# Kernel tuning notes

Hardware: AMD Instinct MI355X
Metric: run time of the kernel (lower is better)

The kernel has to match this reference:

```python
import jax, jax.numpy as jnp
import numpy as np

D = 1024      # input_dim = clip_model.text_projection.shape[1]
P = D // 8    # pre_dim1 == pre_dim2 == 128
B, NS, NT, C = 4096, 8192, 8192, 1000
EPS = 1e-5
SCALE = 0.1
BETA_S = 1.0
BETA_T = 1.0


def setup_inputs() -> dict:
    key = jax.random.key(0)
    ks = jax.random.split(key, 24)
    rn = lambda k, shp, s=0.02: jax.random.normal(k, shp, dtype=jnp.float32) * s
    inp = {
        "Ft": jax.random.normal(ks[0], (C, D), dtype=jnp.float32),
        "Fv": jax.random.normal(ks[1], (B, D), dtype=jnp.float32),
        "Fvs_bank": jax.random.normal(ks[2], (NS, D), dtype=jnp.float32),
        "Fvt_bank": jax.random.normal(ks[3], (NT, D), dtype=jnp.float32),
        # pre_project: Linear(D->P), BN(P), ReLU, Linear(P->P), BN(P), ReLU, Linear(P->3D)
        "W1": rn(ks[4], (P, D)), "b1": jnp.zeros((P,), jnp.float32),
        "g1": jnp.ones((P,), jnp.float32), "be1": jnp.zeros((P,), jnp.float32),
        "m1": jnp.zeros((P,), jnp.float32), "v1": jnp.ones((P,), jnp.float32),
        "W2": rn(ks[5], (P, P)), "b2": jnp.zeros((P,), jnp.float32),
        "g2": jnp.ones((P,), jnp.float32), "be2": jnp.zeros((P,), jnp.float32),
        "m2": jnp.zeros((P,), jnp.float32), "v2": jnp.ones((P,), jnp.float32),
        "W3": rn(ks[6], (3 * D, P)), "b3": jnp.zeros((3 * D,), jnp.float32),
        # post_project: Linear(D->D)
        "Wp": rn(ks[7], (D, D)), "bp": jnp.zeros((D,), jnp.float32),
        "logit_scale": jnp.asarray(np.log(1.0 / 0.07), dtype=jnp.float32),
    }
    return inp


def _pre_project(x, W1, b1, g1, be1, m1, v1, W2, b2, g2, be2, m2, v2, W3, b3):
    # Linear -> BatchNorm1d (eval: running stats) -> ReLU, twice, then Linear to 3*D
    h = x @ W1.T + b1
    h = jax.nn.relu((h - m1) * jax.lax.rsqrt(v1 + EPS) * g1 + be1)
    h = h @ W2.T + b2
    h = jax.nn.relu((h - m2) * jax.lax.rsqrt(v2 + EPS) * g2 + be2)
    return h @ W3.T + b3  # (n, 3*D)


def _qkv(o):
    # einops 'b (d k) -> k b d' with k=3: interleaved split along last dim
    o = o.reshape(o.shape[0], D, 3)
    return o[..., 0], o[..., 1], o[..., 2]


def reference(Ft, Fv, Fvs_bank, Fvt_bank, W1, b1, g1, be1, m1, v1,
              W2, b2, g2, be2, m2, v2, W3, b3, Wp, bp, logit_scale):
    pre = lambda x: _pre_project(x, W1, b1, g1, be1, m1, v1,
                                 W2, b2, g2, be2, m2, v2, W3, b3)
    q_fv, _, _ = _qkv(pre(Fv))
    _, k_fvs, v_fvs = _qkv(pre(Fvs_bank))
    _, k_fvt, v_fvt = _qkv(pre(Fvt_bank))

    As = jax.nn.softmax(SCALE * (q_fv @ k_fvs.T), axis=-1)  # (B, NS)
    At = jax.nn.softmax(SCALE * (q_fv @ k_fvt.T), axis=-1)  # (B, NT)

    Fsa = Fv + (As @ v_fvs) @ Wp.T + bp
    Fta = Fv + (At @ v_fvt) @ Wp.T + bp
    Fsa = Fsa / jnp.linalg.norm(Fsa, axis=-1, keepdims=True)
    Fta = Fta / jnp.linalg.norm(Fta, axis=-1, keepdims=True)

    ls = jnp.exp(logit_scale)
    logits = BETA_S * ls * (Fsa @ Ft.T) + BETA_T * ls * (Fta @ Ft.T)
    return logits  # (B, C)
```

## Files before the change

### kernel.cpp

```cpp
#include <hip/hip_runtime.h>
#include <hip/hip_bf16.h>
#include <math.h>

#define D_DIM   1024
#define P_DIM   128
#define B_ROWS  4096
#define NBANK   8192
#define C_CLS   1000
#define EPS_BN  1e-5f
#define SCALE_S 0.1f
#define MTOT    20480
#define KVSEG   8
#define KCH     64
#define CHUNKS  (NBANK / KVSEG / KCH)

typedef __bf16 bf16x8 __attribute__((ext_vector_type(8)));
typedef float  f32x4  __attribute__((ext_vector_type(4)));
typedef __hip_bfloat16 bf;

__device__ __forceinline__ void load_lds16(const void* gp, void* lp) {
    __builtin_amdgcn_global_load_lds(
        (__attribute__((address_space(1))) void*)gp,
        (__attribute__((address_space(3))) void*)lp, 16, 0, 0);
}

__device__ __forceinline__ int4 pack8(float4 a, float4 b) {
    union { bf h[8]; int4 v; } u;
    u.h[0] = __float2bfloat16(a.x); u.h[1] = __float2bfloat16(a.y);
    u.h[2] = __float2bfloat16(a.z); u.h[3] = __float2bfloat16(a.w);
    u.h[4] = __float2bfloat16(b.x); u.h[5] = __float2bfloat16(b.y);
    u.h[6] = __float2bfloat16(b.z); u.h[7] = __float2bfloat16(b.w);
    return u.v;
}

__global__ __launch_bounds__(256)
void gemm_bf16(const bf* __restrict__ A, const bf* __restrict__ B,
               int M, int N, int K, int lda, int ldb,
               int kchunks, int fx, int fy, int epi,
               float* __restrict__ Cf, bf* __restrict__ Cb,
               const float* __restrict__ bias, const float* __restrict__ biasm,
               const float* __restrict__ bng, const float* __restrict__ bnb,
               const float* __restrict__ bnm, const float* __restrict__ bnv,
               const float* __restrict__ addsrc, const float* __restrict__ lsp,
               int ldc)
{
    __shared__ __align__(16) short ldsS[8192];
    short* lsA = ldsS;
    short* lsB = ldsS + 4096;

    const int tid  = threadIdx.x;
    const int wave = tid >> 6;
    const int lane = tid & 63;
    const int wm   = wave >> 1;
    const int wn   = wave & 1;
    const int r16  = lane & 15;
    const int quad = lane >> 4;

    const int gx = gridDim.x, gy = gridDim.y;
    const int l   = blockIdx.y * gx + blockIdx.x;
    const int xcd = l & 7;
    const int i0  = l >> 3;
    const int sx  = gx / fx, sy = gy / fy;
    const int bx  = (xcd % fx) * sx + (i0 % sx);
    const int by  = (xcd / fx) * sy + (i0 / sx);
    const int bm0 = by * 128;
    const int bn0 = bx * 128;

    const int kper = K / kchunks;
    const int kbeg = blockIdx.z * kper;
    const int kend = kbeg + kper;

    f32x4 acc[4][4];
#pragma unroll
    for (int i = 0; i < 4; ++i)
#pragma unroll
        for (int j = 0; j < 4; ++j) acc[i][j] = (f32x4){0.f, 0.f, 0.f, 0.f};

    for (int k0 = kbeg; k0 < kend; k0 += 32) {
#pragma unroll
        for (int i = 0; i < 2; ++i) {
            const int s   = i * 256 + tid;
            const int row = s >> 2;
            const int cc  = (s & 3) * 8;
            const int lofs = (i * 256 + wave * 64) * 16;
            load_lds16(A + (size_t)(bm0 + row) * lda + k0 + cc, (char*)lsA + lofs);
            load_lds16(B + (size_t)(bn0 + row) * ldb + k0 + cc, (char*)lsB + lofs);
        }
        __syncthreads();

        bf16x8 af[4], bfr[4];
#pragma unroll
        for (int i = 0; i < 4; ++i)
            af[i] = *(const bf16x8*)(lsA + (wm * 64 + i * 16 + r16) * 32 + quad * 8);
#pragma unroll
        for (int j = 0; j < 4; ++j)
            bfr[j] = *(const bf16x8*)(lsB + (wn * 64 + j * 16 + r16) * 32 + quad * 8);
#pragma unroll
        for (int i = 0; i < 4; ++i)
#pragma unroll
            for (int j = 0; j < 4; ++j)
                acc[i][j] = __builtin_amdgcn_mfma_f32_16x16x32_bf16(
                    af[i], bfr[j], acc[i][j], 0, 0, 0);
        __syncthreads();
    }

    if (epi == 3 || epi == 4) {
        const float lsv = (epi == 4) ? expf(*lsp) : 1.0f;
#pragma unroll
        for (int i = 0; i < 4; ++i) {
            const int gmb = bm0 + wm * 64 + i * 16 + quad * 4;
#pragma unroll
            for (int j = 0; j < 4; ++j) {
                const int gn = bn0 + wn * 64 + j * 16 + r16;
#pragma unroll
                for (int r = 0; r < 4; ++r) {
                    const int gm = gmb + r;
                    float val = acc[i][j][r];
                    if (epi == 3) {
                        Cf[(size_t)gm * N + gn] =
                            val + bias[gn] + addsrc[(size_t)(gm & (ldc - 1)) * N + gn];
                    } else {
                        if (gn < ldc) Cf[(size_t)gm * ldc + gn] = val * lsv;
                    }
                }
            }
        }
        return;
    }

    bf* dst = Cb + (epi == 6 ? (size_t)blockIdx.z * M * N : 0);
    bf* my  = (bf*)(ldsS + wave * 2048);

#pragma unroll
    for (int half = 0; half < 2; ++half) {
#pragma unroll
        for (int i2 = 0; i2 < 2; ++i2) {
            const int i = half * 2 + i2;
            const int gmb = bm0 + wm * 64 + i * 16 + quad * 4;
#pragma unroll
            for (int j = 0; j < 4; ++j) {
                const int gn = bn0 + wn * 64 + j * 16 + r16;
#pragma unroll
                for (int r = 0; r < 4; ++r) {
                    float val = acc[i][j][r];
                    if (epi == 1) {
                        val += bias[gn];
                        val = (val - bnm[gn]) * rsqrtf(bnv[gn] + EPS_BN) * bng[gn] + bnb[gn];
                        val = fmaxf(val, 0.f);
                    } else {
                        if (bias)  val += bias[gn];
                        if (biasm) val += biasm[gmb + r];
                    }
                    my[(i2 * 16 + quad * 4 + r) * 64 + j * 16 + r16] =
                        __float2bfloat16(val);
                }
            }
        }
#pragma unroll
        for (int it = 0; it < 4; ++it) {
            const int chunk = it * 64 + lane;
            const int lrow  = chunk >> 3;
            const int lcol  = (chunk & 7) * 8;
            const int grow  = bm0 + wm * 64 + half * 32 + lrow;
            const int gcol  = bn0 + wn * 64 + lcol;
            int4 v = *(const int4*)(my + lrow * 64 + lcol);
            *(int4*)(dst + (size_t)grow * N + gcol) = v;
        }
    }
}

__global__ __launch_bounds__(256)
void attn_fused(const bf* __restrict__ qt,
                const bf* __restrict__ h2bank,
                const bf* __restrict__ h2T,
                const float* __restrict__ beta,
                bf* __restrict__ Ypart,
                float* __restrict__ rsP)
{
    __shared__ __align__(16) short lds[40960];
    short* lsQ = lds;
    short* lsK = lds + 16384;
    short* lsV = lds + 24576;
    short* lsS = lds + 32768;

    const int tid  = threadIdx.x;
    const int wave = tid >> 6;
    const int lane = tid & 63;
    const int wm   = wave >> 1;
    const int wn   = wave & 1;
    const int r16  = lane & 15;
    const int quad = lane >> 4;

    const int qb   = blockIdx.x >> 4;
    const int side = (blockIdx.x >> 3) & 1;
    const int seg  = blockIdx.x & 7;
    const int part = side * 8 + seg;
    const int nseg0 = seg * (NBANK / KVSEG);
    const bf* kbase = h2bank + (size_t)side * NBANK * P_DIM;
    const int ncol0 = side * NBANK;

#pragma unroll
    for (int m = 0; m < 8; ++m) {
        const int s = m * 256 + tid;
        const int row = s >> 4, pcg = s & 15;
        const int lcg = pcg ^ (row & 15);
        load_lds16(qt + (size_t)(qb * 128 + row) * 128 + lcg * 8,
                   (char*)lsQ + (m * 256 + wave * 64) * 16);
    }

    f32x4 sacc[4][2], yacc[4][4];
    float rsacc[4][4];
#pragma unroll
    for (int i = 0; i < 4; ++i) {
#pragma unroll
        for (int j = 0; j < 4; ++j) yacc[i][j] = (f32x4){0.f, 0.f, 0.f, 0.f};
#pragma unroll
        for (int j = 0; j < 2; ++j) sacc[i][j] = (f32x4){0.f, 0.f, 0.f, 0.f};
#pragma unroll
        for (int r = 0; r < 4; ++r) rsacc[i][r] = 0.f;
    }

    for (int c = 0; c < CHUNKS; ++c) {
        const int kv0 = nseg0 + c * KCH;
        __syncthreads();
#pragma unroll
        for (int m = 0; m < 4; ++m) {
            const int s = m * 256 + tid;
            const int row = s >> 4, pcg = s & 15;
            const int lcg = pcg ^ (row & 15);
            load_lds16(kbase + (size_t)(kv0 + row) * P_DIM + lcg * 8,
                       (char*)lsK + (m * 256 + wave * 64) * 16);
        }
#pragma unroll
        for (int m = 0; m < 4; ++m) {
            const int s = m * 256 + tid;
            const int row = s >> 3, pcg = s & 7;
            const int lcg = pcg ^ (row & 7);
            load_lds16(h2T + (size_t)row * (2 * NBANK) + ncol0 + kv0 + lcg * 8,
                       (char*)lsV + (m * 256 + wave * 64) * 16);
        }
        __syncthreads();

#pragma unroll
        for (int ks = 0; ks < 4; ++ks) {
            bf16x8 af[4], bfr[2];
#pragma unroll
            for (int i = 0; i < 4; ++i) {
                const int qr = wm * 64 + i * 16 + r16;
                af[i] = *(const bf16x8*)(lsQ + qr * 128 +
                                         ((ks * 4 + quad) ^ (qr & 15)) * 8);
            }
#pragma unroll
            for (int j = 0; j < 2; ++j) {
                const int kr = wn * 32 + j * 16 + r16;
                bfr[j] = *(const bf16x8*)(lsK + kr * 128 +
                                          ((ks * 4 + quad) ^ (kr & 15)) * 8);
            }
#pragma unroll
            for (int i = 0; i < 4; ++i)
#pragma unroll
                for (int j = 0; j < 2; ++j)
                    sacc[i][j] = __builtin_amdgcn_mfma_f32_16x16x32_bf16(
                        af[i], bfr[j], sacc[i][j], 0, 0, 0);
        }

#pragma unroll
        for (int j = 0; j < 2; ++j) {
            const int col = wn * 32 + j * 16 + r16;
            const float bv = beta[(size_t)side * NBANK + kv0 + col];
            const int cg = col >> 3, cl = col & 7;
#pragma unroll
            for (int i = 0; i < 4; ++i) {
#pragma unroll
                for (int r = 0; r < 4; ++r) {
                    const int row = wm * 64 + i * 16 + quad * 4 + r;
                    float v = __expf(SCALE_S * (sacc[i][j][r] + bv));
                    rsacc[i][r] += v;
                    ((bf*)lsS)[row * 64 + ((cg ^ (row & 7)) << 3) + cl] =
                        __float2bfloat16(v);
                }
            }
        }
#pragma unroll
        for (int i = 0; i < 4; ++i)
#pragma unroll
            for (int j = 0; j < 2; ++j) sacc[i][j] = (f32x4){0.f, 0.f, 0.f, 0.f};

        __syncthreads();

#pragma unroll
        for (int ks = 0; ks < 2; ++ks) {
            bf16x8 pa[4], pb[4];
#pragma unroll
            for (int i = 0; i < 4; ++i) {
                const int sr = wm * 64 + i * 16 + r16;
                pa[i] = *(const bf16x8*)(lsS + sr * 64 +
                                         ((ks * 4 + quad) ^ (sr & 7)) * 8);
            }
#pragma unroll
            for (int j = 0; j < 4; ++j) {
                const int vr = wn * 64 + j * 16 + r16;
                pb[j] = *(const bf16x8*)(lsV + vr * 64 +
                                         ((ks * 4 + quad) ^ (vr & 7)) * 8);
            }
#pragma unroll
            for (int i = 0; i < 4; ++i)
#pragma unroll
                for (int j = 0; j < 4; ++j)
                    yacc[i][j] = __builtin_amdgcn_mfma_f32_16x16x32_bf16(
                        pa[i], pb[j], yacc[i][j], 0, 0, 0);
        }
    }

    __syncthreads();
    float* frs = (float*)lsK;
#pragma unroll
    for (int i = 0; i < 4; ++i)
#pragma unroll
        for (int r = 0; r < 4; ++r) {
            float s = rsacc[i][r];
            s += __shfl_xor(s, 1, 64);
            s += __shfl_xor(s, 2, 64);
            s += __shfl_xor(s, 4, 64);
            s += __shfl_xor(s, 8, 64);
            if (r16 == 0) frs[wn * 128 + wm * 64 + i * 16 + quad * 4 + r] = s;
        }
    __syncthreads();
    if (tid < 128)
        rsP[(size_t)part * B_ROWS + qb * 128 + tid] = frs[tid] + frs[128 + tid];
    __syncthreads();

    bf* my  = (bf*)(lds + 16384) + wave * 2048;
    bf* dst = Ypart + (size_t)part * B_ROWS * P_DIM;
#pragma unroll
    for (int half = 0; half < 2; ++half) {
#pragma unroll
        for (int i2 = 0; i2 < 2; ++i2) {
            const int i = half * 2 + i2;
#pragma unroll
            for (int j = 0; j < 4; ++j)
#pragma unroll
                for (int r = 0; r < 4; ++r)
                    my[(i2 * 16 + quad * 4 + r) * 64 + j * 16 + r16] =
                        __float2bfloat16(yacc[i][j][r]);
        }
#pragma unroll
        for (int it = 0; it < 4; ++it) {
            const int chunk = it * 64 + lane;
            const int lrow  = chunk >> 3;
            const int lcol  = (chunk & 7) * 8;
            const int grow  = qb * 128 + wm * 64 + half * 32 + lrow;
            const int gcol  = wn * 64 + lcol;
            int4 v = *(const int4*)(my + lrow * 64 + lcol);
            *(int4*)(dst + (size_t)grow * P_DIM + gcol) = v;
        }
    }
}

#define PG0 10240
#define PG1 584
#define PG2 64
#define PG3 512
#define PG4 8
#define PG5 256

__global__ __launch_bounds__(256)
void prep(const float* __restrict__ Fv, const float* __restrict__ Fvs,
          const float* __restrict__ Fvt,
          const float* __restrict__ W1, const float* __restrict__ W2,
          const float* __restrict__ Wp,
          const float* __restrict__ W3, const float* __restrict__ b3,
          const float* __restrict__ bp, const float* __restrict__ Ft,
          bf* __restrict__ Xb, bf* __restrict__ W1b, bf* __restrict__ W2b,
          bf* __restrict__ Wpb,
          bf* __restrict__ Tq, bf* __restrict__ Tk, bf* __restrict__ Tv,
          bf* __restrict__ Ftb,
          float* __restrict__ vvecP, float* __restrict__ bvp)
{
    const int tid = threadIdx.x;
    int b = blockIdx.x;
    if (b < PG0) {
        int i = (b * 256 + tid) * 8;
        const int n0 = B_ROWS * D_DIM, n1 = n0 + NBANK * D_DIM;
        const float* src; int off;
        if (i < n0)      { src = Fv;  off = i; }
        else if (i < n1) { src = Fvs; off = i - n0; }
        else             { src = Fvt; off = i - n1; }
        float4 a = *(const float4*)(src + off);
        float4 c = *(const float4*)(src + off + 4);
        *(int4*)(Xb + i) = pack8(a, c);
        return;
    }
    if ((b -= PG0) < PG1) {
        int i = (b * 256 + tid) * 8;
        const int n1 = P_DIM * D_DIM, n2 = n1 + P_DIM * P_DIM;
        const float* src; bf* dst; int off;
        if (i < n1)      { src = W1; dst = W1b; off = i; }
        else if (i < n2) { src = W2; dst = W2b; off = i - n1; }
        else             { src = Wp; dst = Wpb; off = i - n2; }
        float4 a = *(const float4*)(src + off);
        float4 c = *(const float4*)(src + off + 4);
        *(int4*)(dst + off) = pack8(a, c);
        return;
    }
    if ((b -= PG1) < PG2) {
        int i = (b * 256 + tid) * 8;
        int p = i >> 10, d0 = i & 1023;
        union { bf h[8]; int4 v; } uq, uk, uv;
#pragma unroll
        for (int j = 0; j < 8; ++j) {
            const float* r = W3 + (size_t)3 * (d0 + j) * P_DIM + p;
            uq.h[j] = __float2bfloat16(r[0]);
            uk.h[j] = __float2bfloat16(r[P_DIM]);
            uv.h[j] = __float2bfloat16(r[2 * P_DIM]);
        }
        *(int4*)(Tq + i) = uq.v;
        *(int4*)(Tk + i) = uk.v;
        *(int4*)(Tv + i) = uv.v;
        return;
    }
    if ((b -= PG2) < PG3) {
        int i = (b * 256 + tid) * 8;
        int row = i >> 10, col = i & 1023;
        if (row < C_CLS) {
            float4 a = *(const float4*)(Ft + (size_t)row * D_DIM + col);
            float4 c = *(const float4*)(Ft + (size_t)row * D_DIM + col + 4);
            *(int4*)(Ftb + i) = pack8(a, c);
        } else {
            *(int4*)(Ftb + i) = (int4){0, 0, 0, 0};
        }
        return;
    }
    if ((b -= PG3) < PG4) {
        const int p = tid & 127, hf = tid >> 7;
        const int dbase = b * 128 + hf * 64;
        float s = 0.f;
        for (int dd = 0; dd < 64; ++dd) {
            const int d = dbase + dd;
            s = fmaf(b3[3 * d], W3[(size_t)(3 * d + 1) * P_DIM + p], s);
        }
        vvecP[(b * 2 + hf) * P_DIM + p] = s;
        return;
    }
    b -= PG4;
    const int wave = tid >> 6, lane = tid & 63;
    const int o = b * 4 + wave;
    const float* r = Wp + (size_t)o * D_DIM;
    float s = 0.f;
    for (int i = lane; i < D_DIM; i += 64) s = fmaf(r[i], b3[3 * i + 2], s);
    for (int off = 32; off > 0; off >>= 1) s += __shfl_down(s, off, 64);
    if (lane == 0) bvp[o] = s + bp[o];
}

__global__ __launch_bounds__(256)
void reduceWW(const bf* __restrict__ WqkP, const bf* __restrict__ WpvP,
              bf* __restrict__ Wqk, bf* __restrict__ Wpv)
{
    const int tid = threadIdx.x;
    if (blockIdx.x < 8) {
        int i = (blockIdx.x * 256 + tid) * 8;
        float s[8] = {};
        for (int z = 0; z < 8; ++z) {
            union { int4 v; bf h[8]; } u;
            u.v = *(const int4*)(WqkP + (size_t)z * 16384 + i);
#pragma unroll
            for (int e = 0; e < 8; ++e) s[e] += __bfloat162float(u.h[e]);
        }
        union { bf h[8]; int4 v; } o;
#pragma unroll
        for (int e = 0; e < 8; ++e) o.h[e] = __float2bfloat16(s[e]);
        *(int4*)(Wqk + i) = o.v;
    } else {
        int i = ((blockIdx.x - 8) * 256 + tid) * 8;
        float s[8] = {};
        for (int z = 0; z < 4; ++z) {
            union { int4 v; bf h[8]; } u;
            u.v = *(const int4*)(WpvP + (size_t)z * 131072 + i);
#pragma unroll
            for (int e = 0; e < 8; ++e) s[e] += __bfloat162float(u.h[e]);
        }
        union { bf h[8]; int4 v; } o;
#pragma unroll
        for (int e = 0; e < 8; ++e) o.h[e] = __float2bfloat16(s[e]);
        *(int4*)(Wpv + i) = o.v;
    }
}

__global__ __launch_bounds__(256)
void posth2(const bf* __restrict__ h2bank, const float* __restrict__ vvecP,
            float* __restrict__ beta, bf* __restrict__ h2T)
{
    __shared__ float vs[P_DIM];
    __shared__ bf t[64][136];
    const int tid = threadIdx.x;
    if (blockIdx.x < 64) {
        if (tid < P_DIM) {
            float s = 0.f;
#pragma unroll
            for (int z = 0; z < 16; ++z) s += vvecP[z * P_DIM + tid];
            vs[tid] = s;
        }
        __syncthreads();
        const int n = blockIdx.x * 256 + tid;
        const bf* r = h2bank + (size_t)n * P_DIM;
        float s = 0.f;
#pragma unroll
        for (int c = 0; c < P_DIM; c += 8) {
            union { int4 q; bf h[8]; } u;
            u.q = *(const int4*)(r + c);
#pragma unroll
            for (int e = 0; e < 8; ++e) s += __bfloat162float(u.h[e]) * vs[c + e];
        }
        beta[n] = s;
    } else {
        const size_t n0 = (size_t)(blockIdx.x - 64) * 64;
#pragma unroll
        for (int q = 0; q < 4; ++q) {
            int idx = (q * 256 + tid) * 8;
            int r = idx >> 7, c = idx & 127;
            *(int4*)&t[r][c] = *(const int4*)(h2bank + (n0 + r) * P_DIM + c);
        }
        __syncthreads();
        const int p  = tid >> 1;
        const int nb = (tid & 1) * 32;
#pragma unroll
        for (int q = 0; q < 4; ++q) {
            const int n = nb + q * 8;
            union { int4 v; bf h[8]; } u;
#pragma unroll
            for (int e = 0; e < 8; ++e) u.h[e] = t[n + e][p];
            *(int4*)(h2T + (size_t)p * (2 * NBANK) + n0 + n) = u.v;
        }
    }
}

__global__ __launch_bounds__(256)
void reduceY(const bf* __restrict__ parts, const float* __restrict__ rsP,
             bf* __restrict__ Yhat)
{
    int j = (blockIdx.x * 256 + threadIdx.x) * 8;
    const int s = j >> 19;
    const int qrow = (j >> 7) & (B_ROWS - 1);
    float rs = 0.f;
#pragma unroll
    for (int g = 0; g < 8; ++g)
        rs += rsP[(size_t)(s * 8 + g) * B_ROWS + qrow];
    const bf* p = parts + (size_t)s * 8 * 524288 + (size_t)(j & 524287);
    float acc[8] = {};
    for (int z = 0; z < 8; ++z) {
        union { int4 v; bf h[8]; } u;
        u.v = *(const int4*)(p + (size_t)z * 524288);
#pragma unroll
        for (int e = 0; e < 8; ++e) acc[e] += __bfloat162float(u.h[e]);
    }
    const float inv = 1.0f / rs;
    union { bf h[8]; int4 v; } o;
#pragma unroll
    for (int e = 0; e < 8; ++e) o.h[e] = __float2bfloat16(acc[e] * inv);
    *(int4*)(Yhat + j) = o.v;
}

__global__ __launch_bounds__(256)
void rownorm2b(const float* __restrict__ G, bf* __restrict__ out)
{
    __shared__ float red[16];
    const int tid = threadIdx.x;
    const float* ps = G + (size_t)blockIdx.x * D_DIM;
    const float* pt = ps + (size_t)B_ROWS * D_DIM;
    float4 a = *(const float4*)(ps + tid * 4);
    float4 c = *(const float4*)(pt + tid * 4);
    float sa = a.x * a.x + a.y * a.y + a.z * a.z + a.w * a.w;
    float sb = c.x * c.x + c.y * c.y + c.z * c.z + c.w * c.w;
    for (int s = 32; s > 0; s >>= 1) {
        sa += __shfl_down(sa, s, 64);
        sb += __shfl_down(sb, s, 64);
    }
    if ((tid & 63) == 0) { red[tid >> 6] = sa; red[8 + (tid >> 6)] = sb; }
    __syncthreads();
    if (tid == 0) {
        float ta = 0.f, tb = 0.f;
        for (int w = 0; w < 4; ++w) { ta += red[w]; tb += red[8 + w]; }
        red[4] = rsqrtf(ta); red[12] = rsqrtf(tb);
    }
    __syncthreads();
    const float ia = red[4], ib = red[12];
    union { bf h[4]; int2 v; } o;
    o.h[0] = __float2bfloat16(a.x * ia + c.x * ib);
    o.h[1] = __float2bfloat16(a.y * ia + c.y * ib);
    o.h[2] = __float2bfloat16(a.z * ia + c.z * ib);
    o.h[3] = __float2bfloat16(a.w * ia + c.w * ib);
    *(int2*)(out + (size_t)blockIdx.x * D_DIM + tid * 4) = o.v;
}

extern "C" void kernel_launch(void* const* d_in, const int* in_sizes, int n_in,
                              void* d_out, int out_size, void* d_ws, size_t ws_size,
                              hipStream_t stream)
{
    (void)in_sizes; (void)n_in; (void)out_size; (void)ws_size;

    const float* Ft  = (const float*)d_in[0];
    const float* Fv  = (const float*)d_in[1];
    const float* Fvs = (const float*)d_in[2];
    const float* Fvt = (const float*)d_in[3];
    const float* W1  = (const float*)d_in[4];
    const float* b1  = (const float*)d_in[5];
    const float* g1  = (const float*)d_in[6];
    const float* be1 = (const float*)d_in[7];
    const float* m1  = (const float*)d_in[8];
    const float* v1  = (const float*)d_in[9];
    const float* W2  = (const float*)d_in[10];
    const float* b2  = (const float*)d_in[11];
    const float* g2  = (const float*)d_in[12];
    const float* be2 = (const float*)d_in[13];
    const float* m2  = (const float*)d_in[14];
    const float* v2  = (const float*)d_in[15];
    const float* W3  = (const float*)d_in[16];
    const float* b3  = (const float*)d_in[17];
    const float* Wp  = (const float*)d_in[18];
    const float* bp  = (const float*)d_in[19];
    const float* ls  = (const float*)d_in[20];

    char* base = (char*)d_ws;
    size_t o = 0;
    auto take = [&](size_t s) { size_t r = o; o += (s + 255) & ~(size_t)255; return r; };

    bf* qtb   = (bf*)(base + take((size_t)B_ROWS * P_DIM * 2));
    bf* h2T   = (bf*)(base + take((size_t)P_DIM * 2 * NBANK * 2));
    bf* Yhat  = (bf*)(base + take((size_t)2 * B_ROWS * P_DIM * 2));
    bf* Wpb   = (bf*)(base + take((size_t)D_DIM * D_DIM * 2));
    bf* Ftb   = (bf*)(base + take((size_t)D_DIM * D_DIM * 2));
    bf* W3qT  = (bf*)(base + take((size_t)P_DIM * D_DIM * 2));
    bf* W3kT  = (bf*)(base + take((size_t)P_DIM * D_DIM * 2));
    bf* W3vT  = (bf*)(base + take((size_t)P_DIM * D_DIM * 2));
    bf* Wqk   = (bf*)(base + take((size_t)P_DIM * P_DIM * 2));
    bf* Wpvb  = (bf*)(base + take((size_t)D_DIM * P_DIM * 2));
    bf* W1b   = (bf*)(base + take((size_t)P_DIM * D_DIM * 2));
    bf* W2b   = (bf*)(base + take((size_t)P_DIM * P_DIM * 2));
    bf* h2b   = (bf*)(base + take((size_t)MTOT * P_DIM * 2));
    bf* WqkP  = (bf*)(base + take((size_t)8 * P_DIM * P_DIM * 2));
    bf* WpvP  = (bf*)(base + take((size_t)4 * D_DIM * P_DIM * 2));
    float* vvecP = (float*)(base + take((size_t)16 * P_DIM * 4));
    float* beta  = (float*)(base + take((size_t)2 * NBANK * 4));
    float* bvp   = (float*)(base + take(D_DIM * 4));
    float* rsP   = (float*)(base + take((size_t)16 * B_ROWS * 4));

    const size_t Dbase = o;
    bf* Xb    = (bf*)(base + Dbase);
    bf* h1b   = (bf*)(base + Dbase + (size_t)MTOT * D_DIM * 2);
    bf* Opart = (bf*)(base + Dbase + (size_t)48 * 1024 * 1024);
    float* G     = (float*)(base + Dbase);
    bf*    Fsumb = (bf*)(base + Dbase + (size_t)2 * B_ROWS * D_DIM * 4);

    auto gemm = [&](const bf* A, const bf* B, int M, int N, int K, int lda, int ldb,
                    int kch, int fx, int fy, int epi, float* Cf, bf* Cb,
                    const float* bias, const float* biasm,
                    const float* bg, const float* bb, const float* bm, const float* bv,
                    const float* addsrc, const float* lsp, int ldc) {
        gemm_bf16<<<dim3(N / 128, M / 128, kch), dim3(256), 0, stream>>>(
            A, B, M, N, K, lda, ldb, kch, fx, fy, epi, Cf, Cb, bias, biasm,
            bg, bb, bm, bv, addsrc, lsp, ldc);
    };

    prep<<<dim3(PG0 + PG1 + PG2 + PG3 + PG4 + PG5), dim3(256), 0, stream>>>(
        Fv, Fvs, Fvt, W1, W2, Wp, W3, b3, bp, Ft,
        Xb, W1b, W2b, Wpb, W3qT, W3kT, W3vT, Ftb, vvecP, bvp);

    gemm(W3kT, W3qT, P_DIM, P_DIM, D_DIM, D_DIM, D_DIM, 8, 1, 1, 6, nullptr, WqkP,
         nullptr, nullptr, nullptr, nullptr, nullptr, nullptr, nullptr, nullptr, 0);
    gemm(Wpb, W3vT, D_DIM, P_DIM, D_DIM, D_DIM, D_DIM, 4, 1, 8, 6, nullptr, WpvP,
         nullptr, nullptr, nullptr, nullptr, nullptr, nullptr, nullptr, nullptr, 0);
    reduceWW<<<dim3(72), dim3(256), 0, stream>>>(WqkP, WpvP, Wqk, Wpvb);

    gemm(Xb, W1b, MTOT, P_DIM, D_DIM, D_DIM, D_DIM, 1, 1, 8, 1, nullptr, h1b,
         b1, nullptr, g1, be1, m1, v1, nullptr, nullptr, 0);
    gemm(h1b, W2b, MTOT, P_DIM, P_DIM, P_DIM, P_DIM, 1, 1, 8, 1, nullptr, h2b,
         b2, nullptr, g2, be2, m2, v2, nullptr, nullptr, 0);
    gemm(h2b, Wqk, B_ROWS, P_DIM, P_DIM, P_DIM, P_DIM, 1, 1, 8, 5, nullptr, qtb,
         nullptr, nullptr, nullptr, nullptr, nullptr, nullptr, nullptr, nullptr, 0);
    posth2<<<dim3(320), dim3(256), 0, stream>>>(
        h2b + (size_t)B_ROWS * P_DIM, vvecP, beta, h2T);

    attn_fused<<<dim3(2 * KVSEG * (B_ROWS / 128)), dim3(256), 0, stream>>>(
        qtb, h2b + (size_t)B_ROWS * P_DIM, h2T, beta, Opart, rsP);
    reduceY<<<dim3(2 * B_ROWS * P_DIM / 2048), dim3(256), 0, stream>>>(
        Opart, rsP, Yhat);

    gemm(Yhat, Wpvb, 2 * B_ROWS, D_DIM, P_DIM, P_DIM, P_DIM, 1, 1, 8, 3, G, nullptr,
         bvp, nullptr, nullptr, nullptr, nullptr, nullptr, Fv, nullptr, B_ROWS);
    rownorm2b<<<dim3(B_ROWS), dim3(256), 0, stream>>>(G, Fsumb);
    gemm(Fsumb, Ftb, B_ROWS, D_DIM, D_DIM, D_DIM, D_DIM, 1, 1, 8, 4, (float*)d_out,
         nullptr, nullptr, nullptr, nullptr, nullptr, nullptr, nullptr, nullptr,
         ls, C_CLS);
}
```

Baseline: 396.9 us.

## Restructure attention kernel to per-wave query rows with Q in registers

The fused attention kernel now runs 512 threads as 8 waves. Each wave owns 16 query rows, keeps its Q fragments in registers and computes the full 64-key score tile and the 128-wide output itself. This drops the Q LDS tile, shrinks LDS use and removes the barrier between writing and reading the score tile, since each wave only touches its own rows. The KV bank is split into twice as many segments to keep the grid large. In exchange, every wave re-reads all of K and V from LDS, so the LDS-to-MFMA ratio gets worse, and reduceY must combine twice as many partial outputs and row sums.

After: 373.7 us. 5.8% less time.

```diff
diff --git a/kernel.cpp b/kernel.cpp
--- a/kernel.cpp
+++ b/kernel.cpp
@@ -10,7 +10,7 @@
 #define EPS_BN  1e-5f
 #define SCALE_S 0.1f
 #define MTOT    20480
-#define KVSEG   8
+#define KVSEG   16
 #define KCH     64
 #define CHUNKS  (NBANK / KVSEG / KCH)
 
@@ -169,7 +169,7 @@
     }
 }
 
-__global__ __launch_bounds__(256)
+__global__ __launch_bounds__(512)
 void attn_fused(const bf* __restrict__ qt,
                 const bf* __restrict__ h2bank,
                 const bf* __restrict__ h2T,
@@ -177,183 +177,139 @@
                 bf* __restrict__ Ypart,
                 float* __restrict__ rsP)
 {
-    __shared__ __align__(16) short lds[40960];
-    short* lsQ = lds;
-    short* lsK = lds + 16384;
-    short* lsV = lds + 24576;
-    short* lsS = lds + 32768;
+    __shared__ __align__(16) short lds[24576];
+    short* lsK = lds;
+    short* lsV = lds + 8192;
+    short* lsS = lds + 16384;
 
     const int tid  = threadIdx.x;
     const int wave = tid >> 6;
     const int lane = tid & 63;
-    const int wm   = wave >> 1;
-    const int wn   = wave & 1;
     const int r16  = lane & 15;
     const int quad = lane >> 4;
 
-    const int qb   = blockIdx.x >> 4;
-    const int side = (blockIdx.x >> 3) & 1;
-    const int seg  = blockIdx.x & 7;
-    const int part = side * 8 + seg;
+    const int qb   = blockIdx.x >> 5;
+    const int side = (blockIdx.x >> 4) & 1;
+    const int seg  = blockIdx.x & 15;
+    const int part = side * KVSEG + seg;
     const int nseg0 = seg * (NBANK / KVSEG);
     const bf* kbase = h2bank + (size_t)side * NBANK * P_DIM;
     const int ncol0 = side * NBANK;
 
-#pragma unroll
-    for (int m = 0; m < 8; ++m) {
-        const int s = m * 256 + tid;
-        const int row = s >> 4, pcg = s & 15;
-        const int lcg = pcg ^ (row & 15);
-        load_lds16(qt + (size_t)(qb * 128 + row) * 128 + lcg * 8,
-                   (char*)lsQ + (m * 256 + wave * 64) * 16);
-    }
-
-    f32x4 sacc[4][2], yacc[4][4];
-    float rsacc[4][4];
-#pragma unroll
-    for (int i = 0; i < 4; ++i) {
-#pragma unroll
-        for (int j = 0; j < 4; ++j) yacc[i][j] = (f32x4){0.f, 0.f, 0.f, 0.f};
-#pragma unroll
-        for (int j = 0; j < 2; ++j) sacc[i][j] = (f32x4){0.f, 0.f, 0.f, 0.f};
-#pragma unroll
-        for (int r = 0; r < 4; ++r) rsacc[i][r] = 0.f;
-    }
+    const bf* qrow = qt + (size_t)(qb * 128 + wave * 16 + r16) * P_DIM;
+    bf16x8 qreg[4];
+#pragma unroll
+    for (int ks = 0; ks < 4; ++ks)
+        qreg[ks] = *(const bf16x8*)(qrow + (ks * 4 + quad) * 8);
+
+    f32x4 yacc[8];
+    float rsacc[4] = {0.f, 0.f, 0.f, 0.f};
+#pragma unroll
+    for (int j = 0; j < 8; ++j) yacc[j] = (f32x4){0.f, 0.f, 0.f, 0.f};
 
     for (int c = 0; c < CHUNKS; ++c) {
         const int kv0 = nseg0 + c * KCH;
         __syncthreads();
 #pragma unroll
-        for (int m = 0; m < 4; ++m) {
-            const int s = m * 256 + tid;
+        for (int m = 0; m < 2; ++m) {
+            const int s = m * 512 + tid;
             const int row = s >> 4, pcg = s & 15;
             const int lcg = pcg ^ (row & 15);
             load_lds16(kbase + (size_t)(kv0 + row) * P_DIM + lcg * 8,
-                       (char*)lsK + (m * 256 + wave * 64) * 16);
-        }
-#pragma unroll
-        for (int m = 0; m < 4; ++m) {
-            const int s = m * 256 + tid;
+                       (char*)lsK + (m * 512 + wave * 64) * 16);
+        }
+#pragma unroll
+        for (int m = 0; m < 2; ++m) {
+            const int s = m * 512 + tid;
             const int row = s >> 3, pcg = s & 7;
             const int lcg = pcg ^ (row & 7);
             load_lds16(h2T + (size_t)row * (2 * NBANK) + ncol0 + kv0 + lcg * 8,
-                       (char*)lsV + (m * 256 + wave * 64) * 16);
+                       (char*)lsV + (m * 512 + wave * 64) * 16);
         }
         __syncthreads();
 
+        f32x4 sacc[4];
+#pragma unroll
+        for (int j = 0; j < 4; ++j) sacc[j] = (f32x4){0.f, 0.f, 0.f, 0.f};
 #pragma unroll
         for (int ks = 0; ks < 4; ++ks) {
-            bf16x8 af[4], bfr[2];
-#pragma unroll
-            for (int i = 0; i < 4; ++i) {
-                const int qr = wm * 64 + i * 16 + r16;
-                af[i] = *(const bf16x8*)(lsQ + qr * 128 +
-                                         ((ks * 4 + quad) ^ (qr & 15)) * 8);
-            }
-#pragma unroll
-            for (int j = 0; j < 2; ++j) {
-                const int kr = wn * 32 + j * 16 + r16;
+            bf16x8 bfr[4];
+#pragma unroll
+            for (int j = 0; j < 4; ++j) {
+                const int kr = j * 16 + r16;
                 bfr[j] = *(const bf16x8*)(lsK + kr * 128 +
                                           ((ks * 4 + quad) ^ (kr & 15)) * 8);
             }
 #pragma unroll
-            for (int i = 0; i < 4; ++i)
-#pragma unroll
-                for (int j = 0; j < 2; ++j)
-                    sacc[i][j] = __builtin_amdgcn_mfma_f32_16x16x32_bf16(
-                        af[i], bfr[j], sacc[i][j], 0, 0, 0);
-        }
-
-#pragma unroll
-        for (int j = 0; j < 2; ++j) {
-            const int col = wn * 32 + j * 16 + r16;
+            for (int j = 0; j < 4; ++j)
+                sacc[j] = __builtin_amdgcn_mfma_f32_16x16x32_bf16(
+                    qreg[ks], bfr[j], sacc[j], 0, 0, 0);
+        }
+
+#pragma unroll
+        for (int j = 0; j < 4; ++j) {
+            const int col = j * 16 + r16;
             const float bv = beta[(size_t)side * NBANK + kv0 + col];
             const int cg = col >> 3, cl = col & 7;
 #pragma unroll
-            for (int i = 0; i < 4; ++i) {
-#pragma unroll
-                for (int r = 0; r < 4; ++r) {
-                    const int row = wm * 64 + i * 16 + quad * 4 + r;
-                    float v = __expf(SCALE_S * (sacc[i][j][r] + bv));
-                    rsacc[i][r] += v;
-                    ((bf*)lsS)[row * 64 + ((cg ^ (row & 7)) << 3) + cl] =
-                        __float2bfloat16(v);
-                }
+            for (int r = 0; r < 4; ++r) {
+                const int row = wave * 16 + quad * 4 + r;
+                float v = __expf(SCALE_S * (sacc[j][r] + bv));
+                rsacc[r] += v;
+                ((bf*)lsS)[row * 64 + ((cg ^ (row & 7)) << 3) + cl] =
+                    __float2bfloat16(v);
             }
         }
-#pragma unroll
-        for (int i = 0; i < 4; ++i)
-#pragma unroll
-            for (int j = 0; j < 2; ++j) sacc[i][j] = (f32x4){0.f, 0.f, 0.f, 0.f};
-
-        __syncthreads();
 
 #pragma unroll
         for (int ks = 0; ks < 2; ++ks) {
-            bf16x8 pa[4], pb[4];
-#pragma unroll
-            for (int i = 0; i < 4; ++i) {
-                const int sr = wm * 64 + i * 16 + r16;
-                pa[i] = *(const bf16x8*)(lsS + sr * 64 +
+            const int sr = wave * 16 + r16;
+            bf16x8 pa = *(const bf16x8*)(lsS + sr * 64 +
                                          ((ks * 4 + quad) ^ (sr & 7)) * 8);
-            }
-#pragma unroll
-            for (int j = 0; j < 4; ++j) {
-                const int vr = wn * 64 + j * 16 + r16;
+            bf16x8 pb[8];
+#pragma unroll
+            for (int j = 0; j < 8; ++j) {
+                const int vr = j * 16 + r16;
                 pb[j] = *(const bf16x8*)(lsV + vr * 64 +
                                          ((ks * 4 + quad) ^ (vr & 7)) * 8);
             }
 #pragma unroll
-            for (int i = 0; i < 4; ++i)
-#pragma unroll
-                for (int j = 0; j < 4; ++j)
-                    yacc[i][j] = __builtin_amdgcn_mfma_f32_16x16x32_bf16(
-                        pa[i], pb[j], yacc[i][j], 0, 0, 0);
-        }
-    }
+            for (int j = 0; j < 8; ++j)
+                yacc[j] = __builtin_amdgcn_mfma_f32_16x16x32_bf16(
+                    pa, pb[j], yacc[j], 0, 0, 0);
+        }
+    }
+
+#pragma unroll
+    for (int r = 0; r < 4; ++r) {
+        float s = rsacc[r];
+        s += __shfl_xor(s, 1, 64);
+        s += __shfl_xor(s, 2, 64);
+        s += __shfl_xor(s, 4, 64);
+        s += __shfl_xor(s, 8, 64);
+        rsacc[r] = s;
+    }
+    if (r16 == 0)
+        *(float4*)(rsP + (size_t)part * B_ROWS + qb * 128 + wave * 16 + quad * 4) =
+            (float4){rsacc[0], rsacc[1], rsacc[2], rsacc[3]};
 
     __syncthreads();
-    float* frs = (float*)lsK;
-#pragma unroll
-    for (int i = 0; i < 4; ++i)
-#pragma unroll
-        for (int r = 0; r < 4; ++r) {
-            float s = rsacc[i][r];
-            s += __shfl_xor(s, 1, 64);
-            s += __shfl_xor(s, 2, 64);
-            s += __shfl_xor(s, 4, 64);
-            s += __shfl_xor(s, 8, 64);
-            if (r16 == 0) frs[wn * 128 + wm * 64 + i * 16 + quad * 4 + r] = s;
-        }
-    __syncthreads();
-    if (tid < 128)
-        rsP[(size_t)part * B_ROWS + qb * 128 + tid] = frs[tid] + frs[128 + tid];
-    __syncthreads();
-
-    bf* my  = (bf*)(lds + 16384) + wave * 2048;
-    bf* dst = Ypart + (size_t)part * B_ROWS * P_DIM;
-#pragma unroll
-    for (int half = 0; half < 2; ++half) {
-#pragma unroll
-        for (int i2 = 0; i2 < 2; ++i2) {
-            const int i = half * 2 + i2;
-#pragma unroll
-            for (int j = 0; j < 4; ++j)
-#pragma unroll
-                for (int r = 0; r < 4; ++r)
-                    my[(i2 * 16 + quad * 4 + r) * 64 + j * 16 + r16] =
-                        __float2bfloat16(yacc[i][j][r]);
-        }
-#pragma unroll
-        for (int it = 0; it < 4; ++it) {
-            const int chunk = it * 64 + lane;
-            const int lrow  = chunk >> 3;
-            const int lcol  = (chunk & 7) * 8;
-            const int grow  = qb * 128 + wm * 64 + half * 32 + lrow;
-            const int gcol  = wn * 64 + lcol;
-            int4 v = *(const int4*)(my + lrow * 64 + lcol);
-            *(int4*)(dst + (size_t)grow * P_DIM + gcol) = v;
-        }
+    bf* my = (bf*)lds + wave * 2048;
+#pragma unroll
+    for (int j = 0; j < 8; ++j)
+#pragma unroll
+        for (int r = 0; r < 4; ++r)
+            my[(quad * 4 + r) * 128 + j * 16 + r16] =
+                __float2bfloat16(yacc[j][r]);
+    bf* dst = Ypart + (size_t)part * B_ROWS * P_DIM
+                    + (size_t)(qb * 128 + wave * 16) * P_DIM;
+#pragma unroll
+    for (int it = 0; it < 4; ++it) {
+        const int chunk = it * 64 + lane;
+        const int lrow  = chunk >> 4;
+        const int lcol  = (chunk & 15) * 8;
+        *(int4*)(dst + (size_t)lrow * P_DIM + lcol) =
+            *(const int4*)(my + lrow * 128 + lcol);
     }
 }
 
@@ -543,11 +499,11 @@
     const int qrow = (j >> 7) & (B_ROWS - 1);
     float rs = 0.f;
 #pragma unroll
-    for (int g = 0; g < 8; ++g)
-        rs += rsP[(size_t)(s * 8 + g) * B_ROWS + qrow];
-    const bf* p = parts + (size_t)s * 8 * 524288 + (size_t)(j & 524287);
+    for (int g = 0; g < KVSEG; ++g)
+        rs += rsP[(size_t)(s * KVSEG + g) * B_ROWS + qrow];
+    const bf* p = parts + (size_t)s * KVSEG * 524288 + (size_t)(j & 524287);
     float acc[8] = {};
-    for (int z = 0; z < 8; ++z) {
+    for (int z = 0; z < KVSEG; ++z) {
         union { int4 v; bf h[8]; } u;
         u.v = *(const int4*)(p + (size_t)z * 524288);
 #pragma unroll
@@ -642,7 +598,7 @@
     float* vvecP = (float*)(base + take((size_t)16 * P_DIM * 4));
     float* beta  = (float*)(base + take((size_t)2 * NBANK * 4));
     float* bvp   = (float*)(base + take(D_DIM * 4));
-    float* rsP   = (float*)(base + take((size_t)16 * B_ROWS * 4));
+    float* rsP   = (float*)(base + take((size_t)2 * KVSEG * B_ROWS * 4));
 
     const size_t Dbase = o;
     bf* Xb    = (bf*)(base + Dbase);
@@ -680,7 +636,7 @@
     posth2<<<dim3(320), dim3(256), 0, stream>>>(
         h2b + (size_t)B_ROWS * P_DIM, vvecP, beta, h2T);
 
-    attn_fused<<<dim3(2 * KVSEG * (B_ROWS / 128)), dim3(256), 0, stream>>>(
+    attn_fused<<<dim3(2 * KVSEG * (B_ROWS / 128)), dim3(512), 0, stream>>>(
         qtb, h2b + (size_t)B_ROWS * P_DIM, h2T, beta, Opart, rsP);
     reduceY<<<dim3(2 * B_ROWS * P_DIM / 2048), dim3(256), 0, stream>>>(
         Opart, rsP, Yhat);
```
